# Optimization experiments

Measured on AMD Instinct MI355X. Metric: run time of the kernel, lower is better.

## Reference

```python
import jax, jax.numpy as jnp
import numpy as np

B, S, D_MODEL, D_FF, E, K = 4, 2048, 1024, 4096, 8, 2
CAP_FACTOR = 1.0


def setup_inputs() -> dict:
    key = jax.random.key(0)
    ks = jax.random.split(key, 6)
    std = 0.02
    return {
        "x": jax.random.normal(ks[0], (B, S, D_MODEL), jnp.float32),
        "router_w": jax.random.normal(ks[1], (E, D_MODEL), jnp.float32) * std,  # Linear(d_model,E,bias=False) weight
        "w1": jax.random.normal(ks[2], (E, D_MODEL, D_FF), jnp.float32) * std,
        "b1": jnp.zeros((E, D_FF), jnp.float32),
        "w2": jax.random.normal(ks[3], (E, D_FF, D_MODEL), jnp.float32) * std,
        "b2": jnp.zeros((E, D_MODEL), jnp.float32),
    }


def reference(x, router_w, w1, b1, w2, b2):
    b, s, d = x.shape
    T = b * s
    e = router_w.shape[0]
    capacity = int(CAP_FACTOR * T / e)  # static
    xf = x.reshape(T, d)

    # --- routing ---
    logits = xf @ router_w.T                       # [T,E]
    probs = jax.nn.softmax(logits, axis=-1)
    vals, idx = jax.lax.top_k(probs, K)            # [T,K] values / expert ids
    vals = vals / vals.sum(-1, keepdims=True)

    # dense gate matrix [T,E]; top_k experts are distinct so this is a scatter of K weights per token
    ar = jnp.arange(T)
    gates = jnp.zeros((T, e), x.dtype).at[ar[:, None], idx].add(vals)

    # --- load-balancing loss ---
    counts = jnp.zeros((e,), jnp.float32).at[idx.reshape(-1)].add(1.0)
    ideal = T * K / e
    lb_loss = jnp.sum((counts - ideal) ** 2) / (T ** 2)

    # --- capacity-limited dispatch (first `capacity` tokens in token order per expert) ---
    mask = gates > 0                                               # [T,E]
    order = jnp.argsort(jnp.logical_not(mask), axis=0)[:capacity]  # stable: assigned tokens first, ascending token id -> [cap,E]
    valid = jnp.take_along_axis(mask, order, axis=0)               # [cap,E] token actually assigned & within capacity
    idx_ec = order.T                                               # [E,cap]

    # --- grouped expert MLP ---
    xg = xf[idx_ec]                                                # [E,cap,D]
    h = jax.nn.gelu(jnp.einsum('ecd,edf->ecf', xg, w1) + b1[:, None, :], approximate=False)
    y = jnp.einsum('ecf,efd->ecd', h, w2) + b2[:, None, :]         # [E,cap,D]

    # --- combine (scatter-add with routing weights; dropped/invalid slots get weight 0) ---
    wt = gates[idx_ec, jnp.arange(e)[:, None]] * valid.T           # [E,cap]
    out = jnp.zeros((T, d), x.dtype).at[idx_ec.reshape(-1)].add((y * wt[..., None]).reshape(-1, d))
    return out.reshape(b, s, d), lb_loss
```

## Files before the change

### kernel.cpp

```cpp
#include <hip/hip_runtime.h>
#include <hip/hip_bf16.h>

#define T_TOK 8192
#define DMODEL 1024
#define DFF 4096
#define NEXP 8
#define CAP 1024

typedef __attribute__((ext_vector_type(8))) __bf16 bf16x8;
typedef __attribute__((ext_vector_type(4))) float f32x4;

__device__ __forceinline__ unsigned short f2bf(float f) {
  union { float f; unsigned int u; } v;
  v.f = f;
  return (unsigned short)((v.u + 0x7fffu + ((v.u >> 16) & 1u)) >> 16);
}

__device__ __forceinline__ void load_lds16(const unsigned short* g, unsigned short* l) {
  __builtin_amdgcn_global_load_lds((const __attribute__((address_space(1))) void*)g,
                                   (__attribute__((address_space(3))) void*)l,
                                   16, 0, 0);
}

__global__ void k_convert_x(const float* __restrict__ x, unsigned short* __restrict__ xb) {
  int g = blockIdx.x * 256 + threadIdx.x;
  const float4* s = (const float4*)x;
  float4 a = s[2 * g], b = s[2 * g + 1];
  union { unsigned short h[8]; uint4 v; } o;
  o.h[0] = f2bf(a.x); o.h[1] = f2bf(a.y); o.h[2] = f2bf(a.z); o.h[3] = f2bf(a.w);
  o.h[4] = f2bf(b.x); o.h[5] = f2bf(b.y); o.h[6] = f2bf(b.z); o.h[7] = f2bf(b.w);
  ((uint4*)xb)[g] = o.v;
}

__global__ void k_transpose_cvt(const float* __restrict__ src, unsigned short* __restrict__ dst,
                                int Kd, int Nd) {
  __shared__ unsigned short tile[64][72];
  int e = blockIdx.z;
  size_t k0 = (size_t)blockIdx.y * 64, n0 = (size_t)blockIdx.x * 64;
  int tid = threadIdx.x;
  const float* sb = src + (size_t)e * Kd * Nd;
  int r = tid >> 4, cg = (tid & 15) * 4;
  for (int rr = 0; rr < 4; ++rr) {
    int row = r + rr * 16;
    float4 v = *(const float4*)(sb + (k0 + row) * Nd + n0 + cg);
    tile[row][cg + 0] = f2bf(v.x);
    tile[row][cg + 1] = f2bf(v.y);
    tile[row][cg + 2] = f2bf(v.z);
    tile[row][cg + 3] = f2bf(v.w);
  }
  __syncthreads();
  unsigned short* db = dst + (size_t)e * Nd * Kd;
  int rn = tid >> 3, kg = (tid & 7) * 8;
  for (int rr = 0; rr < 2; ++rr) {
    int nrow = rn + rr * 32;
    union { unsigned short h[8]; uint4 v; } o;
#pragma unroll
    for (int j = 0; j < 8; ++j) o.h[j] = tile[kg + j][nrow];
    *(uint4*)(db + (n0 + nrow) * Kd + k0 + kg) = o.v;
  }
}

__global__ void k_router(const float* __restrict__ x, const float* __restrict__ rw,
                         int* __restrict__ tk_idx, float* __restrict__ tk_w) {
  int wv = threadIdx.x >> 6, lane = threadIdx.x & 63;
  int t = blockIdx.x * 4 + wv;
  const float* xr = x + (size_t)t * DMODEL;
  float acc[NEXP];
#pragma unroll
  for (int e = 0; e < NEXP; ++e) acc[e] = 0.f;
  for (int j = 0; j < DMODEL / 64; ++j) {
    float xv = xr[j * 64 + lane];
#pragma unroll
    for (int e = 0; e < NEXP; ++e) acc[e] += xv * rw[e * DMODEL + j * 64 + lane];
  }
#pragma unroll
  for (int e = 0; e < NEXP; ++e)
    for (int off = 32; off; off >>= 1) acc[e] += __shfl_xor(acc[e], off);
  if (lane == 0) {
    int i0 = 0;
    for (int e = 1; e < NEXP; ++e) if (acc[e] > acc[i0]) i0 = e;
    int i1 = (i0 == 0) ? 1 : 0;
    for (int e = 0; e < NEXP; ++e) if (e != i0 && acc[e] > acc[i1]) i1 = e;
    float ex = expf(acc[i1] - acc[i0]);
    float w0 = 1.f / (1.f + ex);
    float w1 = ex / (1.f + ex);
    tk_idx[2 * t] = i0; tk_idx[2 * t + 1] = i1;
    tk_w[2 * t] = w0;  tk_w[2 * t + 1] = w1;
  }
}

__global__ void k_scan(const int* __restrict__ tk_idx, const float* __restrict__ tk_w,
                       int* __restrict__ etok, float* __restrict__ egate,
                       float* __restrict__ loss_out) {
  __shared__ int wavecnt[16][NEXP];
  __shared__ int waveoff[16][NEXP];
  __shared__ int offs[NEXP];
  __shared__ int ctot[NEXP];
  int tid = threadIdx.x;
  int lane = tid & 63, wv = tid >> 6;
  if (tid < NEXP) offs[tid] = 0;
  for (int i = tid; i < NEXP * CAP; i += 1024) { etok[i] = 0; egate[i] = 0.f; }
  __syncthreads();
  unsigned long long lt = (1ULL << lane) - 1ULL;
  for (int c = 0; c < T_TOK / 1024; ++c) {
    int t = c * 1024 + tid;
    int e0 = tk_idx[2 * t], e1 = tk_idx[2 * t + 1];
    float w0 = tk_w[2 * t], w1 = tk_w[2 * t + 1];
    int p0 = 0, p1 = 0;
#pragma unroll
    for (int e = 0; e < NEXP; ++e) {
      unsigned long long bal = __ballot((e0 == e) || (e1 == e));
      if (e0 == e) p0 = __popcll(bal & lt);
      if (e1 == e) p1 = __popcll(bal & lt);
      if (lane == 0) wavecnt[wv][e] = __popcll(bal);
    }
    __syncthreads();
    if (tid < NEXP) {
      int s = 0;
      for (int w = 0; w < 16; ++w) { waveoff[w][tid] = s; s += wavecnt[w][tid]; }
      ctot[tid] = s;
    }
    __syncthreads();
    int r0 = offs[e0] + waveoff[wv][e0] + p0;
    int r1 = offs[e1] + waveoff[wv][e1] + p1;
    if (r0 < CAP) { etok[e0 * CAP + r0] = t; egate[e0 * CAP + r0] = w0; }
    if (r1 < CAP) { etok[e1 * CAP + r1] = t; egate[e1 * CAP + r1] = w1; }
    __syncthreads();
    if (tid < NEXP) offs[tid] += ctot[tid];
    __syncthreads();
  }
  if (tid == 0) {
    float loss = 0.f;
    for (int e = 0; e < NEXP; ++e) {
      float d = (float)offs[e] - 2048.0f;
      loss += d * d;
    }
    loss_out[0] = loss / (8192.0f * 8192.0f);
  }
}

__global__ __launch_bounds__(256) void k_gemm1(
    const unsigned short* __restrict__ xb, const unsigned short* __restrict__ w1t,
    const float* __restrict__ b1, const int* __restrict__ etok,
    unsigned short* __restrict__ H) {
  __shared__ unsigned short As[128 * 32];
  __shared__ unsigned short Bs[128 * 32];
  int tid = threadIdx.x;
  int lane = tid & 63, wv = tid >> 6;
  int bid = blockIdx.x;
  int e = bid >> 8;
  int r = bid & 255;
  int m0 = (r & 7) * 128, n0 = (r >> 3) * 128;

  const unsigned short* gA[2];
  const unsigned short* gB[2];
  unsigned short* lA[2];
  unsigned short* lB[2];
#pragma unroll
  for (int s = 0; s < 2; ++s) {
    int i = s * 256 + tid;
    int row = i >> 2, cb = (i & 3) * 8;
    int tok = etok[e * CAP + m0 + row];
    gA[s] = xb + (size_t)tok * DMODEL + cb;
    gB[s] = w1t + ((size_t)e * DFF + n0 + row) * DMODEL + cb;
    int wb = (s * 256 + wv * 64) * 8;
    lA[s] = As + wb;
    lB[s] = Bs + wb;
  }

  f32x4 zero = {0.f, 0.f, 0.f, 0.f};
  f32x4 acc[4][4];
#pragma unroll
  for (int mi = 0; mi < 4; ++mi)
#pragma unroll
    for (int ni = 0; ni < 4; ++ni) acc[mi][ni] = zero;

  int wm = (wv >> 1) * 64, wn = (wv & 1) * 64;
  int fr = lane & 15, quad = lane >> 4;
  const unsigned short* pa = As + (wm + fr) * 32 + quad * 8;
  const unsigned short* pb = Bs + (wn + fr) * 32 + quad * 8;

  for (int k0 = 0; k0 < DMODEL; k0 += 32) {
#pragma unroll
    for (int s = 0; s < 2; ++s) {
      load_lds16(gA[s] + k0, lA[s]);
      load_lds16(gB[s] + k0, lB[s]);
    }
    __syncthreads();
    bf16x8 av[4], bv[4];
#pragma unroll
    for (int mi = 0; mi < 4; ++mi) av[mi] = *(const bf16x8*)(pa + mi * 16 * 32);
#pragma unroll
    for (int ni = 0; ni < 4; ++ni) bv[ni] = *(const bf16x8*)(pb + ni * 16 * 32);
#pragma unroll
    for (int mi = 0; mi < 4; ++mi)
#pragma unroll
      for (int ni = 0; ni < 4; ++ni)
        acc[mi][ni] = __builtin_amdgcn_mfma_f32_16x16x32_bf16(av[mi], bv[ni], acc[mi][ni], 0, 0, 0);
    __syncthreads();
  }

#pragma unroll
  for (int ni = 0; ni < 4; ++ni) {
    int col = n0 + wn + ni * 16 + fr;
    float bias = b1[e * DFF + col];
#pragma unroll
    for (int mi = 0; mi < 4; ++mi) {
      int mbase = m0 + wm + mi * 16 + quad * 4;
#pragma unroll
      for (int rr = 0; rr < 4; ++rr) {
        float v = acc[mi][ni][rr] + bias;
        v = 0.5f * v * (1.0f + erff(v * 0.70710678118654752440f));
        H[((size_t)e * CAP + mbase + rr) * DFF + col] = f2bf(v);
      }
    }
  }
}

__global__ __launch_bounds__(256) void k_gemm2(
    const unsigned short* __restrict__ H, const unsigned short* __restrict__ w2t,
    const float* __restrict__ b2, const int* __restrict__ etok,
    const float* __restrict__ egate, float* __restrict__ out) {
  __shared__ unsigned short As[128 * 32];
  __shared__ unsigned short Bs[128 * 32];
  int tid = threadIdx.x;
  int lane = tid & 63, wv = tid >> 6;
  int bid = blockIdx.x;
  int e = bid >> 6;
  int r = bid & 63;
  int m0 = (r & 7) * 128, n0 = (r >> 3) * 128;

  const unsigned short* gA[2];
  const unsigned short* gB[2];
  unsigned short* lA[2];
  unsigned short* lB[2];
#pragma unroll
  for (int s = 0; s < 2; ++s) {
    int i = s * 256 + tid;
    int row = i >> 2, cb = (i & 3) * 8;
    gA[s] = H + ((size_t)e * CAP + m0 + row) * DFF + cb;
    gB[s] = w2t + ((size_t)e * DMODEL + n0 + row) * DFF + cb;
    int wb = (s * 256 + wv * 64) * 8;
    lA[s] = As + wb;
    lB[s] = Bs + wb;
  }

  f32x4 zero = {0.f, 0.f, 0.f, 0.f};
  f32x4 acc[4][4];
#pragma unroll
  for (int mi = 0; mi < 4; ++mi)
#pragma unroll
    for (int ni = 0; ni < 4; ++ni) acc[mi][ni] = zero;

  int wm = (wv >> 1) * 64, wn = (wv & 1) * 64;
  int fr = lane & 15, quad = lane >> 4;
  const unsigned short* pa = As + (wm + fr) * 32 + quad * 8;
  const unsigned short* pb = Bs + (wn + fr) * 32 + quad * 8;

  for (int k0 = 0; k0 < DFF; k0 += 32) {
#pragma unroll
    for (int s = 0; s < 2; ++s) {
      load_lds16(gA[s] + k0, lA[s]);
      load_lds16(gB[s] + k0, lB[s]);
    }
    __syncthreads();
    bf16x8 av[4], bv[4];
#pragma unroll
    for (int mi = 0; mi < 4; ++mi) av[mi] = *(const bf16x8*)(pa + mi * 16 * 32);
#pragma unroll
    for (int ni = 0; ni < 4; ++ni) bv[ni] = *(const bf16x8*)(pb + ni * 16 * 32);
#pragma unroll
    for (int mi = 0; mi < 4; ++mi)
#pragma unroll
      for (int ni = 0; ni < 4; ++ni)
        acc[mi][ni] = __builtin_amdgcn_mfma_f32_16x16x32_bf16(av[mi], bv[ni], acc[mi][ni], 0, 0, 0);
    __syncthreads();
  }

  float bs[4];
  int cols[4];
#pragma unroll
  for (int ni = 0; ni < 4; ++ni) {
    cols[ni] = n0 + wn + ni * 16 + fr;
    bs[ni] = b2[e * DMODEL + cols[ni]];
  }
#pragma unroll
  for (int mi = 0; mi < 4; ++mi) {
    int mbase = m0 + wm + mi * 16 + quad * 4;
#pragma unroll
    for (int rr = 0; rr < 4; ++rr) {
      int mrow = mbase + rr;
      int tok = etok[e * CAP + mrow];
      float g = egate[e * CAP + mrow];
      if (g != 0.f) {
        float* orow = out + (size_t)tok * DMODEL;
#pragma unroll
        for (int ni = 0; ni < 4; ++ni)
          atomicAdd(orow + cols[ni], g * (acc[mi][ni][rr] + bs[ni]));
      }
    }
  }
}

extern "C" void kernel_launch(void* const* d_in, const int* in_sizes, int n_in,
                              void* d_out, int out_size, void* d_ws, size_t ws_size,
                              hipStream_t stream) {
  (void)in_sizes; (void)n_in; (void)ws_size;
  const float* x  = (const float*)d_in[0];
  const float* rw = (const float*)d_in[1];
  const float* w1 = (const float*)d_in[2];
  const float* b1 = (const float*)d_in[3];
  const float* w2 = (const float*)d_in[4];
  const float* b2 = (const float*)d_in[5];
  float* out = (float*)d_out;

  char* ws = (char*)d_ws;
  const size_t XB_BYTES = (size_t)T_TOK * DMODEL * 2;
  const size_t WT_BYTES = (size_t)NEXP * DFF * DMODEL * 2;
  const size_t H_BYTES  = (size_t)NEXP * CAP * DFF * 2;
  unsigned short* xb = (unsigned short*)ws;
  unsigned short* wT = (unsigned short*)(ws + XB_BYTES);
  unsigned short* Hb = (unsigned short*)(ws + XB_BYTES + WT_BYTES);
  char* small = ws + XB_BYTES + WT_BYTES + H_BYTES;
  int*   etok  = (int*)small;
  float* egate = (float*)(small + NEXP * CAP * 4);
  int*   tkidx = (int*)(small + 2 * NEXP * CAP * 4);
  float* tkw   = (float*)(small + 2 * NEXP * CAP * 4 + T_TOK * 2 * 4);

  hipMemsetAsync(d_out, 0, (size_t)out_size * sizeof(float), stream);
  k_convert_x<<<(T_TOK * DMODEL / 8) / 256, 256, 0, stream>>>(x, xb);
  k_router<<<T_TOK / 4, 256, 0, stream>>>(x, rw, tkidx, tkw);
  k_scan<<<1, 1024, 0, stream>>>(tkidx, tkw, etok, egate,
                                 (float*)d_out + (size_t)T_TOK * DMODEL);
  k_transpose_cvt<<<dim3(DFF / 64, DMODEL / 64, NEXP), 256, 0, stream>>>(w1, wT, DMODEL, DFF);
  k_gemm1<<<NEXP * 256, 256, 0, stream>>>(xb, wT, b1, etok, Hb);
  k_transpose_cvt<<<dim3(DMODEL / 64, DFF / 64, NEXP), 256, 0, stream>>>(w2, wT, DFF, DMODEL);
  k_gemm2<<<NEXP * 64, 256, 0, stream>>>(Hb, wT, b2, etok, egate, out);
}
```

Baseline: 621.2 us.

## Fuse x conversion into router, stage GEMM1 epilogue through LDS, use fast GELU

The bf16 conversion of x moves into the router kernel, which already reads x, so one full pass over the activations and one launch go away. The router now uses float4 loads. GEMM1's epilogue swaps the MFMA operands, which transposes the accumulator layout so each lane holds 4 consecutive columns. It then stages the bf16 results in LDS and writes them as coalesced 16-byte rows, and replaces erff with a polynomial erf approximation. Block-to-tile mappings are reordered for cache locality, and the transpose tile padding changes to 73. The trade-offs are a small loss of GELU accuracy (the Abramowitz-Stegun erf has about 1e-7 error) and extra LDS traffic in the epilogue.

```diff
diff --git a/kernel.cpp b/kernel.cpp
--- a/kernel.cpp
+++ b/kernel.cpp
@@ -16,25 +16,64 @@
   return (unsigned short)((v.u + 0x7fffu + ((v.u >> 16) & 1u)) >> 16);
 }
 
+__device__ __forceinline__ float fast_gelu(float v) {
+  float x = fabsf(v) * 0.70710678118654752440f;
+  float t = __builtin_amdgcn_rcpf(1.0f + 0.3275911f * x);
+  float poly = t * (0.254829592f + t * (-0.284496736f + t * (1.421413741f +
+               t * (-1.453152027f + t * 1.061405429f))));
+  float er = 1.0f - poly * __expf(-x * x);
+  float s = (v >= 0.0f) ? er : -er;
+  return 0.5f * v * (1.0f + s);
+}
+
 __device__ __forceinline__ void load_lds16(const unsigned short* g, unsigned short* l) {
   __builtin_amdgcn_global_load_lds((const __attribute__((address_space(1))) void*)g,
                                    (__attribute__((address_space(3))) void*)l,
                                    16, 0, 0);
 }
 
-__global__ void k_convert_x(const float* __restrict__ x, unsigned short* __restrict__ xb) {
-  int g = blockIdx.x * 256 + threadIdx.x;
-  const float4* s = (const float4*)x;
-  float4 a = s[2 * g], b = s[2 * g + 1];
-  union { unsigned short h[8]; uint4 v; } o;
-  o.h[0] = f2bf(a.x); o.h[1] = f2bf(a.y); o.h[2] = f2bf(a.z); o.h[3] = f2bf(a.w);
-  o.h[4] = f2bf(b.x); o.h[5] = f2bf(b.y); o.h[6] = f2bf(b.z); o.h[7] = f2bf(b.w);
-  ((uint4*)xb)[g] = o.v;
+__global__ void k_router(const float* __restrict__ x, const float* __restrict__ rw,
+                         unsigned short* __restrict__ xb,
+                         int* __restrict__ tk_idx, float* __restrict__ tk_w) {
+  int wv = threadIdx.x >> 6, lane = threadIdx.x & 63;
+  int t = blockIdx.x * 4 + wv;
+  const float4* xr = (const float4*)(x + (size_t)t * DMODEL);
+  uint2* xbw = (uint2*)(xb + (size_t)t * DMODEL);
+  float acc[NEXP];
+#pragma unroll
+  for (int e = 0; e < NEXP; ++e) acc[e] = 0.f;
+#pragma unroll
+  for (int j = 0; j < DMODEL / 256; ++j) {
+    float4 v = xr[j * 64 + lane];
+#pragma unroll
+    for (int e = 0; e < NEXP; ++e) {
+      float4 w = ((const float4*)(rw + e * DMODEL))[j * 64 + lane];
+      acc[e] += v.x * w.x + v.y * w.y + v.z * w.z + v.w * w.w;
+    }
+    uint2 p;
+    p.x = (unsigned int)f2bf(v.x) | ((unsigned int)f2bf(v.y) << 16);
+    p.y = (unsigned int)f2bf(v.z) | ((unsigned int)f2bf(v.w) << 16);
+    xbw[j * 64 + lane] = p;
+  }
+#pragma unroll
+  for (int e = 0; e < NEXP; ++e)
+    for (int off = 32; off; off >>= 1) acc[e] += __shfl_xor(acc[e], off);
+  if (lane == 0) {
+    int i0 = 0;
+    for (int e = 1; e < NEXP; ++e) if (acc[e] > acc[i0]) i0 = e;
+    int i1 = (i0 == 0) ? 1 : 0;
+    for (int e = 0; e < NEXP; ++e) if (e != i0 && acc[e] > acc[i1]) i1 = e;
+    float ex = expf(acc[i1] - acc[i0]);
+    float w0 = 1.f / (1.f + ex);
+    float w1 = ex / (1.f + ex);
+    tk_idx[2 * t] = i0; tk_idx[2 * t + 1] = i1;
+    tk_w[2 * t] = w0;  tk_w[2 * t + 1] = w1;
+  }
 }
 
 __global__ void k_transpose_cvt(const float* __restrict__ src, unsigned short* __restrict__ dst,
                                 int Kd, int Nd) {
-  __shared__ unsigned short tile[64][72];
+  __shared__ unsigned short tile[64][73];
   int e = blockIdx.z;
   size_t k0 = (size_t)blockIdx.y * 64, n0 = (size_t)blockIdx.x * 64;
   int tid = threadIdx.x;
@@ -57,35 +96,6 @@
 #pragma unroll
     for (int j = 0; j < 8; ++j) o.h[j] = tile[kg + j][nrow];
     *(uint4*)(db + (n0 + nrow) * Kd + k0 + kg) = o.v;
-  }
-}
-
-__global__ void k_router(const float* __restrict__ x, const float* __restrict__ rw,
-                         int* __restrict__ tk_idx, float* __restrict__ tk_w) {
-  int wv = threadIdx.x >> 6, lane = threadIdx.x & 63;
-  int t = blockIdx.x * 4 + wv;
-  const float* xr = x + (size_t)t * DMODEL;
-  float acc[NEXP];
-#pragma unroll
-  for (int e = 0; e < NEXP; ++e) acc[e] = 0.f;
-  for (int j = 0; j < DMODEL / 64; ++j) {
-    float xv = xr[j * 64 + lane];
-#pragma unroll
-    for (int e = 0; e < NEXP; ++e) acc[e] += xv * rw[e * DMODEL + j * 64 + lane];
-  }
-#pragma unroll
-  for (int e = 0; e < NEXP; ++e)
-    for (int off = 32; off; off >>= 1) acc[e] += __shfl_xor(acc[e], off);
-  if (lane == 0) {
-    int i0 = 0;
-    for (int e = 1; e < NEXP; ++e) if (acc[e] > acc[i0]) i0 = e;
-    int i1 = (i0 == 0) ? 1 : 0;
-    for (int e = 0; e < NEXP; ++e) if (e != i0 && acc[e] > acc[i1]) i1 = e;
-    float ex = expf(acc[i1] - acc[i0]);
-    float w0 = 1.f / (1.f + ex);
-    float w1 = ex / (1.f + ex);
-    tk_idx[2 * t] = i0; tk_idx[2 * t + 1] = i1;
-    tk_w[2 * t] = w0;  tk_w[2 * t + 1] = w1;
   }
 }
 
@@ -143,14 +153,16 @@
     const unsigned short* __restrict__ xb, const unsigned short* __restrict__ w1t,
     const float* __restrict__ b1, const int* __restrict__ etok,
     unsigned short* __restrict__ H) {
-  __shared__ unsigned short As[128 * 32];
-  __shared__ unsigned short Bs[128 * 32];
+  __shared__ unsigned short smem[4 * 64 * 72];
+  unsigned short* As = smem;
+  unsigned short* Bs = smem + 4096;
   int tid = threadIdx.x;
   int lane = tid & 63, wv = tid >> 6;
   int bid = blockIdx.x;
   int e = bid >> 8;
-  int r = bid & 255;
-  int m0 = (r & 7) * 128, n0 = (r >> 3) * 128;
+  int b = bid & 255;
+  int nl = b & 7, m = (b >> 3) & 7, nh = b >> 6;
+  int m0 = m * 128, n0 = (nh * 8 + nl) * 128;
 
   const unsigned short* gA[2];
   const unsigned short* gB[2];
@@ -196,24 +208,32 @@
     for (int mi = 0; mi < 4; ++mi)
 #pragma unroll
       for (int ni = 0; ni < 4; ++ni)
-        acc[mi][ni] = __builtin_amdgcn_mfma_f32_16x16x32_bf16(av[mi], bv[ni], acc[mi][ni], 0, 0, 0);
-    __syncthreads();
-  }
-
+        acc[mi][ni] = __builtin_amdgcn_mfma_f32_16x16x32_bf16(bv[ni], av[mi], acc[mi][ni], 0, 0, 0);
+    __syncthreads();
+  }
+
+  unsigned short* L = smem + wv * (64 * 72);
 #pragma unroll
   for (int ni = 0; ni < 4; ++ni) {
-    int col = n0 + wn + ni * 16 + fr;
-    float bias = b1[e * DFF + col];
+    float4 b4 = *(const float4*)(b1 + e * DFF + n0 + wn + ni * 16 + quad * 4);
 #pragma unroll
     for (int mi = 0; mi < 4; ++mi) {
-      int mbase = m0 + wm + mi * 16 + quad * 4;
-#pragma unroll
-      for (int rr = 0; rr < 4; ++rr) {
-        float v = acc[mi][ni][rr] + bias;
-        v = 0.5f * v * (1.0f + erff(v * 0.70710678118654752440f));
-        H[((size_t)e * CAP + mbase + rr) * DFF + col] = f2bf(v);
-      }
-    }
+      float v0 = fast_gelu(acc[mi][ni][0] + b4.x);
+      float v1 = fast_gelu(acc[mi][ni][1] + b4.y);
+      float v2 = fast_gelu(acc[mi][ni][2] + b4.z);
+      float v3 = fast_gelu(acc[mi][ni][3] + b4.w);
+      uint2 p;
+      p.x = (unsigned int)f2bf(v0) | ((unsigned int)f2bf(v1) << 16);
+      p.y = (unsigned int)f2bf(v2) | ((unsigned int)f2bf(v3) << 16);
+      *(uint2*)(L + (mi * 16 + fr) * 72 + ni * 16 + quad * 4) = p;
+    }
+  }
+  int crow = lane >> 3, cchunk = lane & 7;
+#pragma unroll
+  for (int t = 0; t < 8; ++t) {
+    int row = t * 8 + crow;
+    uint4 v = *(const uint4*)(L + row * 72 + cchunk * 8);
+    *(uint4*)(H + ((size_t)e * CAP + m0 + wm + row) * DFF + n0 + wn + cchunk * 8) = v;
   }
 }
 
@@ -227,8 +247,8 @@
   int lane = tid & 63, wv = tid >> 6;
   int bid = blockIdx.x;
   int e = bid >> 6;
-  int r = bid & 63;
-  int m0 = (r & 7) * 128, n0 = (r >> 3) * 128;
+  int b = bid & 63;
+  int m0 = (b >> 3) * 128, n0 = (b & 7) * 128;
 
   const unsigned short* gA[2];
   const unsigned short* gB[2];
@@ -328,8 +348,7 @@
   float* tkw   = (float*)(small + 2 * NEXP * CAP * 4 + T_TOK * 2 * 4);
 
   hipMemsetAsync(d_out, 0, (size_t)out_size * sizeof(float), stream);
-  k_convert_x<<<(T_TOK * DMODEL / 8) / 256, 256, 0, stream>>>(x, xb);
-  k_router<<<T_TOK / 4, 256, 0, stream>>>(x, rw, tkidx, tkw);
+  k_router<<<T_TOK / 4, 256, 0, stream>>>(x, rw, xb, tkidx, tkw);
   k_scan<<<1, 1024, 0, stream>>>(tkidx, tkw, etok, egate,
                                  (float*)d_out + (size_t)T_TOK * DMODEL);
   k_transpose_cvt<<<dim3(DFF / 64, DMODEL / 64, NEXP), 256, 0, stream>>>(w1, wT, DMODEL, DFF);
```

After: 579.1 us. 6.8% less time.
